# Kernel tuning notes

Measured on AMD Instinct MI355X. Metric: run time of the kernel, lower is better.

Reference implementation:

```python
import jax, jax.numpy as jnp
import numpy as np

EPS = 1e-5

def group_points(feat, idx):
    # feat: [B, C, N1], idx: [B, N2, K] -> [B, C, N2, K]
    return jax.vmap(lambda f, i: f[:, i])(feat, idx)

def conv_bn_relu(x, W, gamma, beta):
    # 1x1 conv2d (no bias) + training-mode BatchNorm2d + ReLU
    y = jnp.einsum('oc,bcnk->bonk', W, x)
    mean = y.mean(axis=(0, 2, 3), keepdims=True)
    var = y.var(axis=(0, 2, 3), keepdims=True)  # biased, as BN uses for normalization
    y = (y - mean) * jax.lax.rsqrt(var + EPS)
    y = y * gamma[None, :, None, None] + beta[None, :, None, None]
    return jax.nn.relu(y)

def setup_inputs() -> dict:
    key = jax.random.key(0)
    ks = jax.random.split(key, 12)
    B, N1, N2, K, C1 = 16, 4096, 1024, 32, 64
    mlp = [C1 + 3, 64, 64, 128]  # use_xyz adds 3 channels
    inp = {
        'in_xyz': jax.random.normal(ks[0], (B, 3, N1), jnp.float32),
        'out_xyz': jax.random.normal(ks[1], (B, 3, N2), jnp.float32),
        'in_feature': jax.random.normal(ks[2], (B, C1, N1), jnp.float32),
        'nbr_index': jax.random.randint(ks[3], (B, N2, K), 0, N1, jnp.int32),
    }
    for li in range(3):
        cin, cout = mlp[li], mlp[li + 1]
        inp[f'W{li}'] = jax.random.normal(ks[4 + li], (cout, cin), jnp.float32) * (1.0 / np.sqrt(cin))
        inp[f'g{li}'] = jnp.ones((cout,), jnp.float32)
        inp[f'b{li}'] = jnp.zeros((cout,), jnp.float32)
    return inp

def reference(in_xyz, out_xyz, in_feature, nbr_index,
              W0, g0, b0, W1, g1, b1, W2, g2, b2):
    # gather neighbor features: [B, C1, N2, K]
    nbr_feature = group_points(in_feature, nbr_index)
    # gather neighbor xyz, recenter on query points: [B, 3, N2, K]
    nbr_xyz = group_points(in_xyz, nbr_index) - out_xyz[:, :, :, None]
    x = jnp.concatenate([nbr_feature, nbr_xyz], axis=1)  # [B, C1+3, N2, K]
    x = conv_bn_relu(x, W0, g0, b0)
    x = conv_bn_relu(x, W1, g1, b1)
    x = conv_bn_relu(x, W2, g2, b2)
    return jnp.max(x, axis=3)  # [B, C2, N2]
```

## Files before the change

### kernel.cpp

```cpp
#include <hip/hip_runtime.h>
#include <cstdint>

typedef unsigned short u16;
typedef unsigned int   u32;
typedef __attribute__((ext_vector_type(8))) short  short8;
typedef __attribute__((ext_vector_type(4))) float  floatx4;
typedef __attribute__((ext_vector_type(4))) unsigned int u32x4;

#define NPTS 524288
#define NREP 4

__device__ __forceinline__ float b2f(u16 h) { return __uint_as_float(((u32)h) << 16); }
__device__ __forceinline__ u16 f2b(float f) {
  u32 u = __float_as_uint(f);
  return (u16)((u + 0x7FFFu + ((u >> 16) & 1u)) >> 16);
}
__device__ __forceinline__ u32 pk_bf16(float lo, float hi) {
  return (u32)f2b(lo) | ((u32)f2b(hi) << 16);
}
__device__ __forceinline__ short8 ld_frag8(const u16* p) {
  union { uint4 q; short8 s; } x;
  x.q = *(const uint4*)p;
  return x.s;
}
__device__ __forceinline__ short8 u4_to_s8(uint4 q) {
  union { uint4 q; short8 s; } x; x.q = q; return x.s;
}
__device__ __forceinline__ u32x4 nt_ld4(const void* p) {
  return __builtin_nontemporal_load((const u32x4*)p);
}

__global__ __launch_bounds__(256) void prep_all(const float* __restrict__ inf,
                                                const float* __restrict__ ixyz,
                                                const float* __restrict__ W0,
                                                const float* __restrict__ W1,
                                                const float* __restrict__ W2,
                                                u16* __restrict__ featT,
                                                u16* __restrict__ xyzB,
                                                u16* __restrict__ Wb,
                                                float* __restrict__ gz) {
  __shared__ float tile[32 * 33];
  const int bk = blockIdx.x, t = threadIdx.x;
  if (bk < 4096) {
    int b = bk >> 8, rem = bk & 255, cc = rem >> 7, nc = rem & 127;
    #pragma unroll
    for (int i = 0; i < 4; ++i) {
      int flat = t + i * 256;
      int cl = flat >> 5, nl = flat & 31;
      tile[cl * 33 + nl] = inf[(size_t)((b * 64) + cc * 32 + cl) * 4096 + nc * 32 + nl];
    }
    __syncthreads();
    #pragma unroll
    for (int i = 0; i < 4; ++i) {
      int flat = t + i * 256;
      int nl = flat >> 5, cl = flat & 31;
      featT[(size_t)((b << 12) + nc * 32 + nl) * 64 + cc * 32 + cl] = f2b(tile[cl * 33 + nl]);
    }
  } else if (bk < 4352) {
    int g = (bk - 4096) * 256 + t;
    int b = g >> 12, n = g & 4095;
    const float* p = ixyz + (size_t)b * 12288;
    u32 lo = pk_bf16(p[n], p[4096 + n]);
    u32 hi = (u32)f2b(p[8192 + n]);
    *(uint2*)(xyzB + (size_t)g * 4) = make_uint2(lo, hi);
  } else if (bk < 4432) {
    int s = (bk - 4352) * 256 + t;
    u16 v = 0;
    if (s < 6656)       { int o = s / 104, c = s % 104; if (c < 67) v = f2b(W0[o * 67 + c]); }
    else if (s < 11264) { int q = s - 6656;  int o = q / 72, c = q % 72; if (c < 64) v = f2b(W1[o * 64 + c]); }
    else                { int q = s - 11264; int o = q / 72, c = q % 72; if (c < 64) v = f2b(W2[o * 64 + c]); }
    Wb[s] = v;
  } else {
    #pragma unroll
    for (int i = 0; i < 8; ++i) gz[t + i * 256] = 0.f;
  }
}

template<int KSTEPS, int OCH, bool GATHER, bool MAXOUT>
__global__ __launch_bounds__(256, MAXOUT ? 4 : 5) void gemm_layer(
    const u16* __restrict__ xsrc, const u16* __restrict__ xyzB,
    const float* __restrict__ oxyz, const int* __restrict__ nbr,
    const u16* __restrict__ Wb,
    const float* __restrict__ gsin, const float* __restrict__ gam,
    const float* __restrict__ bet,
    u16* __restrict__ yout, u32* __restrict__ gm,
    float* __restrict__ gsout) {
  constexpr int PITCH = KSTEPS * 32 + 8;
  __shared__ __align__(16) u16 wsh[OCH * PITCH];
  __shared__ float red[512];
  __shared__ float ss[GATHER ? 4 : 128];
  __shared__ float corr[GATHER ? 8 : 1][64];
  __shared__ __align__(16) u32 xt[MAXOUT ? 256 : 2304];

  const int t = threadIdx.x;
  const int blk = (blockIdx.x & 7) * 256 + (blockIdx.x >> 3);
  const int lane = t & 63, wv = t >> 6, lr = lane & 15, quad = lane >> 4;
  const int P0 = blk * 256;
  const int b = blk >> 7;

  {
    const u32* src = (const u32*)Wb;
    u32* dst = (u32*)wsh;
    constexpr int NW = OCH * PITCH / 2;
    #pragma unroll
    for (int i = 0; i < NW / 256; ++i) dst[t + i * 256] = src[t + i * 256];
  }
  if constexpr (GATHER) {
    #pragma unroll
    for (int half = 0; half < 2; ++half) {
      int e = t + half * 256, nn = e >> 6, och = e & 63;
      int n2 = (blk * 8 + nn) & 1023;
      float c = 0.f;
      #pragma unroll
      for (int k = 0; k < 3; ++k)
        c += b2f(Wb[och * 104 + 64 + k]) * oxyz[((b * 3 + k) << 10) + n2];
      corr[nn][och] = c;
    }
  } else {
    if (t < 64) {
      float a = 0.f, q = 0.f;
      #pragma unroll
      for (int rep = 0; rep < NREP; ++rep) {
        a += gsin[rep * 128 + t];
        q += gsin[rep * 128 + 64 + t];
      }
      const float invN = 1.f / (float)NPTS;
      float mean = a * invN;
      float var  = fmaxf(q * invN - mean * mean, 0.f);
      float sc = gam[t] * rsqrtf(var + 1e-5f);
      ss[t] = sc; ss[64 + t] = bet[t] - mean * sc;
    }
  }
  __syncthreads();

  float scr[2][8], shr[2][8];
  if constexpr (!GATHER) {
    #pragma unroll
    for (int ks = 0; ks < 2; ++ks)
      #pragma unroll
      for (int i = 0; i < 8; ++i) {
        const int c = ks * 32 + quad * 8 + i;
        scr[ks][i] = ss[c]; shr[ks][i] = ss[64 + c];
      }
  }

  float s1[4] = {0.f, 0.f, 0.f, 0.f}, s2[4] = {0.f, 0.f, 0.f, 0.f};
  u32* yo = (u32*)yout;

  if constexpr (!MAXOUT) {
    const u16* bp = wsh + lr * PITCH + quad * 8;
    #pragma unroll
    for (int sub = 0; sub < 4; ++sub) {
      const int R = P0 + sub * 64 + wv * 16 + lr;
      short8 av[KSTEPS];
      if constexpr (GATHER) {
        const int id = __builtin_nontemporal_load(&nbr[R]);
        const u16* row = xsrc + (size_t)((b << 12) + id) * 64;
        uint4 a0 = *(const uint4*)(row + quad * 8);
        uint4 a1 = *(const uint4*)(row + quad * 8 + 32);
        u32 w0 = 0u, w1 = 0u;
        if (quad == 0) {
          uint2 v = *(const uint2*)(xyzB + (size_t)((b << 12) + id) * 4);
          w0 = v.x; w1 = v.y;
        }
        av[0] = u4_to_s8(a0);
        av[1] = u4_to_s8(a1);
        av[2] = u4_to_s8(make_uint4(w0, w1, 0u, 0u));
      } else {
        const u16* row = xsrc + ((size_t)R << 6);
        #pragma unroll
        for (int ks = 0; ks < KSTEPS; ++ks) {
          u32x4 raw = nt_ld4(row + ks * 32 + quad * 8);
          u32 w[4] = { raw[0], raw[1], raw[2], raw[3] };
          u32 o[4];
          #pragma unroll
          for (int j = 0; j < 4; ++j) {
            float lo = fmaxf(b2f((u16)(w[j] & 0xffffu)) * scr[ks][2 * j]     + shr[ks][2 * j],     0.f);
            float hi = fmaxf(b2f((u16)(w[j] >> 16))     * scr[ks][2 * j + 1] + shr[ks][2 * j + 1], 0.f);
            o[j] = pk_bf16(lo, hi);
          }
          av[ks] = u4_to_s8(make_uint4(o[0], o[1], o[2], o[3]));
        }
      }
      floatx4 acc[4];
      #pragma unroll
      for (int nt = 0; nt < 4; ++nt) acc[nt] = (floatx4){0.f, 0.f, 0.f, 0.f};
      #pragma unroll
      for (int ks = 0; ks < KSTEPS; ++ks)
        #pragma unroll
        for (int nt = 0; nt < 4; ++nt) {
          short8 bv = ld_frag8(bp + nt * 16 * PITCH + ks * 32);
          acc[nt] = __builtin_amdgcn_mfma_f32_16x16x32_bf16(av[ks], bv, acc[nt], 0, 0, 0);
        }
      float corrv[4] = {0.f, 0.f, 0.f, 0.f};
      if constexpr (GATHER) {
        const int nn = sub * 2 + (wv >> 1);
        #pragma unroll
        for (int nt = 0; nt < 4; ++nt) corrv[nt] = corr[nn][nt * 16 + lr];
      }
      #pragma unroll
      for (int nt = 0; nt < 4; ++nt)
        #pragma unroll
        for (int r = 0; r < 4; ++r) {
          float v = acc[nt][r] - corrv[nt];
          s1[nt] += v; s2[nt] += v * v;
          float vo = __shfl_xor(v, 1);
          if ((lr & 1) == 0)
            xt[(wv * 16 + quad * 4 + r) * 36 + nt * 8 + (lr >> 1)] = pk_bf16(v, vo);
        }
      __syncthreads();
      #pragma unroll
      for (int j = 0; j < 2; ++j) {
        int flat = t + j * 256;
        int rowb = flat >> 3, c4 = flat & 7;
        u32x4 q = *(const u32x4*)&xt[rowb * 36 + c4 * 4];
        __builtin_nontemporal_store(q, (u32x4*)&yo[(size_t)(P0 + sub * 64 + rowb) * 32 + c4 * 4]);
      }
      __syncthreads();
    }
  } else {
    const int rg = wv >> 1, cg = wv & 1;
    const u16* bp = wsh + (cg * 64 + lr) * PITCH + quad * 8;
    u32* gmt = xt + wv * 64;
    for (int sub = 0; sub < 4; ++sub) {
      short8 av[2][2];
      #pragma unroll
      for (int h = 0; h < 2; ++h) {
        const int R = P0 + sub * 64 + rg * 32 + h * 16 + lr;
        const u16* row = xsrc + ((size_t)R << 6);
        #pragma unroll
        for (int ks = 0; ks < 2; ++ks) {
          u32x4 raw = nt_ld4(row + ks * 32 + quad * 8);
          u32 w[4] = { raw[0], raw[1], raw[2], raw[3] };
          u32 o[4];
          #pragma unroll
          for (int j = 0; j < 4; ++j) {
            float lo = fmaxf(b2f((u16)(w[j] & 0xffffu)) * scr[ks][2 * j]     + shr[ks][2 * j],     0.f);
            float hi = fmaxf(b2f((u16)(w[j] >> 16))     * scr[ks][2 * j + 1] + shr[ks][2 * j + 1], 0.f);
            o[j] = pk_bf16(lo, hi);
          }
          av[h][ks] = u4_to_s8(make_uint4(o[0], o[1], o[2], o[3]));
        }
      }
      floatx4 acc[2][4];
      #pragma unroll
      for (int h = 0; h < 2; ++h)
        #pragma unroll
        for (int nt = 0; nt < 4; ++nt) acc[h][nt] = (floatx4){0.f, 0.f, 0.f, 0.f};
      #pragma unroll
      for (int ks = 0; ks < 2; ++ks)
        #pragma unroll
        for (int nt = 0; nt < 4; ++nt) {
          short8 bv = ld_frag8(bp + nt * 16 * PITCH + ks * 32);
          #pragma unroll
          for (int h = 0; h < 2; ++h)
            acc[h][nt] = __builtin_amdgcn_mfma_f32_16x16x32_bf16(av[h][ks], bv, acc[h][nt], 0, 0, 0);
        }
      float mx[4], mn[4];
      #pragma unroll
      for (int nt = 0; nt < 4; ++nt) {
        mx[nt] = -INFINITY; mn[nt] = INFINITY;
        #pragma unroll
        for (int h = 0; h < 2; ++h)
          #pragma unroll
          for (int r = 0; r < 4; ++r) {
            float v = acc[h][nt][r];
            s1[nt] += v; s2[nt] += v * v;
            mx[nt] = fmaxf(mx[nt], v); mn[nt] = fminf(mn[nt], v);
          }
        mx[nt] = fmaxf(mx[nt], __shfl_xor(mx[nt], 16));
        mx[nt] = fmaxf(mx[nt], __shfl_xor(mx[nt], 32));
        mn[nt] = fminf(mn[nt], __shfl_xor(mn[nt], 16));
        mn[nt] = fminf(mn[nt], __shfl_xor(mn[nt], 32));
      }
      if (lane < 16) {
        #pragma unroll
        for (int nt = 0; nt < 4; ++nt)
          gmt[nt * 16 + lane] = pk_bf16(mx[nt], mn[nt]);
      }
      __syncthreads();
      const int grp = blk * 8 + sub * 2 + rg;
      gm[(size_t)grp * 128 + cg * 64 + lane] = gmt[lane];
      __syncthreads();
    }
  }

  #pragma unroll
  for (int nt = 0; nt < 4; ++nt) {
    s1[nt] += __shfl_xor(s1[nt], 16); s1[nt] += __shfl_xor(s1[nt], 32);
    s2[nt] += __shfl_xor(s2[nt], 16); s2[nt] += __shfl_xor(s2[nt], 32);
  }
  if (lane < 16) {
    #pragma unroll
    for (int nt = 0; nt < 4; ++nt) {
      red[wv * 64 + nt * 16 + lr] = s1[nt];
      red[256 + wv * 64 + nt * 16 + lr] = s2[nt];
    }
  }
  __syncthreads();
  float* gb = gsout + (blk & (NREP - 1)) * (MAXOUT ? 256 : 128);
  if constexpr (!MAXOUT) {
    if (t < 64) {
      unsafeAtomicAdd(&gb[t], red[t] + red[64 + t] + red[128 + t] + red[192 + t]);
    } else if (t < 128) {
      int c = t - 64;
      unsafeAtomicAdd(&gb[64 + c], red[256 + c] + red[320 + c] + red[384 + c] + red[448 + c]);
    }
  } else {
    if (t < 128) {
      int half = t >> 6, i = t & 63;
      unsafeAtomicAdd(&gb[t], red[half * 64 + i] + red[(half + 2) * 64 + i]);
    } else {
      int c = t - 128, half = c >> 6, i = c & 63;
      unsafeAtomicAdd(&gb[128 + c], red[256 + half * 64 + i] + red[256 + (half + 2) * 64 + i]);
    }
  }
}

__global__ __launch_bounds__(256) void final_out(const u32* __restrict__ gm,
                                                 const float* __restrict__ gs,
                                                 const float* __restrict__ gam,
                                                 const float* __restrict__ bet,
                                                 float* __restrict__ out) {
  __shared__ float tile[64 * 33];
  __shared__ float ssc[128], ssh[128];
  int blk = blockIdx.x;
  int b = blk >> 6, rem = blk & 63, cc = rem >> 4, nn = rem & 15;
  int t = threadIdx.x;
  if (t < 128) {
    float a = 0.f, q = 0.f;
    #pragma unroll
    for (int rep = 0; rep < NREP; ++rep) {
      a += gs[rep * 256 + t];
      q += gs[rep * 256 + 128 + t];
    }
    const float invN = 1.f / (float)NPTS;
    float mean = a * invN;
    float var  = fmaxf(q * invN - mean * mean, 0.f);
    float sc = gam[t] * rsqrtf(var + 1e-5f);
    ssc[t] = sc; ssh[t] = bet[t] - mean * sc;
  }
  __syncthreads();
  #pragma unroll
  for (int i = 0; i < 8; ++i) {
    int flat = t + i * 256;
    int n2l = flat >> 5, cl = flat & 31;
    int c = cc * 32 + cl;
    size_t idx = (size_t)((b << 10) + nn * 64 + n2l) * 128 + c;
    u32 p = gm[idx];
    float mxv = b2f((u16)(p & 0xffffu)), mnv = b2f((u16)(p >> 16));
    float scv = ssc[c], shv = ssh[c];
    float v = (scv >= 0.f) ? mxv : mnv;
    tile[n2l * 33 + cl] = fmaxf(scv * v + shv, 0.f);
  }
  __syncthreads();
  #pragma unroll
  for (int i = 0; i < 8; ++i) {
    int flat = t + i * 256;
    int cl = flat >> 6, n2l = flat & 63;
    out[(size_t)((b * 128) + cc * 32 + cl) * 1024 + nn * 64 + n2l] = tile[n2l * 33 + cl];
  }
}

extern "C" void kernel_launch(void* const* d_in, const int* in_sizes, int n_in,
                              void* d_out, int out_size, void* d_ws, size_t ws_size,
                              hipStream_t stream) {
  const float* in_xyz  = (const float*)d_in[0];
  const float* out_xyz = (const float*)d_in[1];
  const float* in_feat = (const float*)d_in[2];
  const int*   nbr     = (const int*)d_in[3];
  const float* W0 = (const float*)d_in[4];
  const float* g0 = (const float*)d_in[5];
  const float* b0 = (const float*)d_in[6];
  const float* W1 = (const float*)d_in[7];
  const float* g1 = (const float*)d_in[8];
  const float* b1 = (const float*)d_in[9];
  const float* W2 = (const float*)d_in[10];
  const float* g2 = (const float*)d_in[11];
  const float* b2 = (const float*)d_in[12];
  float* out = (float*)d_out;

  char* ws = (char*)d_ws;
  u16*    Wb    = (u16*)(ws + 4096);
  float*  gs0   = (float*)(ws + 49152);
  float*  gs1   = (float*)(ws + 51200);
  float*  gs2   = (float*)(ws + 53248);
  u16*    featT = (u16*)(ws + 262144);
  u16*    xyzB  = (u16*)(ws + 8650752);
  u16*    y0    = (u16*)(ws + 9699328);
  u16*    y1    = (u16*)(ws + 76808192);
  u32*    gm    = (u32*)(ws + 9699328);

  hipLaunchKernelGGL(prep_all, dim3(4433), dim3(256), 0, stream,
                     in_feat, in_xyz, W0, W1, W2, featT, xyzB, Wb, gs0);

  hipLaunchKernelGGL((gemm_layer<3, 64, true, false>), dim3(2048), dim3(256), 0, stream,
                     featT, xyzB, out_xyz, nbr, Wb, nullptr, nullptr, nullptr,
                     y0, nullptr, gs0);

  hipLaunchKernelGGL((gemm_layer<2, 64, false, false>), dim3(2048), dim3(256), 0, stream,
                     y0, nullptr, nullptr, nullptr, Wb + 6656, gs0, g0, b0,
                     y1, nullptr, gs1);

  hipLaunchKernelGGL((gemm_layer<2, 128, false, true>), dim3(2048), dim3(256), 0, stream,
                     y1, nullptr, nullptr, nullptr, Wb + 11264, gs1, g1, b1,
                     nullptr, gm, gs2);

  hipLaunchKernelGGL(final_out, dim3(1024), dim3(256), 0, stream, gm, gs2, g2, b2, out);
}
```

Baseline: 214.9 us.

## Prefetch all sub-tile input rows up front and use lightweight LDS barriers

```diff
diff --git a/kernel.cpp b/kernel.cpp
--- a/kernel.cpp
+++ b/kernel.cpp
@@ -28,6 +28,9 @@
 }
 __device__ __forceinline__ u32x4 nt_ld4(const void* p) {
   return __builtin_nontemporal_load((const u32x4*)p);
+}
+__device__ __forceinline__ void bar_lds() {
+  asm volatile("s_waitcnt lgkmcnt(0)\n\ts_barrier" ::: "memory");
 }
 
 __global__ __launch_bounds__(256) void prep_all(const float* __restrict__ inf,
@@ -149,29 +152,42 @@
 
   if constexpr (!MAXOUT) {
     const u16* bp = wsh + lr * PITCH + quad * 8;
+    uint4 ga[4][2]; uint2 gx[4]; u32x4 raw[4][2];
+    if constexpr (GATHER) {
+      int idx4[4];
+      #pragma unroll
+      for (int sub = 0; sub < 4; ++sub)
+        idx4[sub] = __builtin_nontemporal_load(&nbr[P0 + sub * 64 + wv * 16 + lr]);
+      #pragma unroll
+      for (int sub = 0; sub < 4; ++sub) {
+        const u16* row = xsrc + (size_t)((b << 12) + idx4[sub]) * 64;
+        ga[sub][0] = *(const uint4*)(row + quad * 8);
+        ga[sub][1] = *(const uint4*)(row + quad * 8 + 32);
+        if (quad == 0)
+          gx[sub] = *(const uint2*)(xyzB + (size_t)((b << 12) + idx4[sub]) * 4);
+      }
+    } else {
+      #pragma unroll
+      for (int sub = 0; sub < 4; ++sub) {
+        const u16* row = xsrc + ((size_t)(P0 + sub * 64 + wv * 16 + lr) << 6);
+        #pragma unroll
+        for (int ks = 0; ks < 2; ++ks)
+          raw[sub][ks] = nt_ld4(row + ks * 32 + quad * 8);
+      }
+    }
     #pragma unroll
     for (int sub = 0; sub < 4; ++sub) {
-      const int R = P0 + sub * 64 + wv * 16 + lr;
       short8 av[KSTEPS];
       if constexpr (GATHER) {
-        const int id = __builtin_nontemporal_load(&nbr[R]);
-        const u16* row = xsrc + (size_t)((b << 12) + id) * 64;
-        uint4 a0 = *(const uint4*)(row + quad * 8);
-        uint4 a1 = *(const uint4*)(row + quad * 8 + 32);
         u32 w0 = 0u, w1 = 0u;
-        if (quad == 0) {
-          uint2 v = *(const uint2*)(xyzB + (size_t)((b << 12) + id) * 4);
-          w0 = v.x; w1 = v.y;
-        }
-        av[0] = u4_to_s8(a0);
-        av[1] = u4_to_s8(a1);
+        if (quad == 0) { w0 = gx[sub].x; w1 = gx[sub].y; }
+        av[0] = u4_to_s8(ga[sub][0]);
+        av[1] = u4_to_s8(ga[sub][1]);
         av[2] = u4_to_s8(make_uint4(w0, w1, 0u, 0u));
       } else {
-        const u16* row = xsrc + ((size_t)R << 6);
-        #pragma unroll
-        for (int ks = 0; ks < KSTEPS; ++ks) {
-          u32x4 raw = nt_ld4(row + ks * 32 + quad * 8);
-          u32 w[4] = { raw[0], raw[1], raw[2], raw[3] };
+        #pragma unroll
+        for (int ks = 0; ks < 2; ++ks) {
+          u32 w[4] = { raw[sub][ks][0], raw[sub][ks][1], raw[sub][ks][2], raw[sub][ks][3] };
           u32 o[4];
           #pragma unroll
           for (int j = 0; j < 4; ++j) {
@@ -208,30 +224,38 @@
           if ((lr & 1) == 0)
             xt[(wv * 16 + quad * 4 + r) * 36 + nt * 8 + (lr >> 1)] = pk_bf16(v, vo);
         }
-      __syncthreads();
+      bar_lds();
       #pragma unroll
       for (int j = 0; j < 2; ++j) {
         int flat = t + j * 256;
         int rowb = flat >> 3, c4 = flat & 7;
         u32x4 q = *(const u32x4*)&xt[rowb * 36 + c4 * 4];
-        __builtin_nontemporal_store(q, (u32x4*)&yo[(size_t)(P0 + sub * 64 + rowb) * 32 + c4 * 4]);
-      }
-      __syncthreads();
+        *(u32x4*)&yo[(size_t)(P0 + sub * 64 + rowb) * 32 + c4 * 4] = q;
+      }
+      bar_lds();
     }
   } else {
     const int rg = wv >> 1, cg = wv & 1;
     const u16* bp = wsh + (cg * 64 + lr) * PITCH + quad * 8;
     u32* gmt = xt + wv * 64;
+    u32x4 raw[4][2][2];
+    #pragma unroll
+    for (int sub = 0; sub < 4; ++sub)
+      #pragma unroll
+      for (int h = 0; h < 2; ++h) {
+        const u16* row = xsrc + ((size_t)(P0 + sub * 64 + rg * 32 + h * 16 + lr) << 6);
+        #pragma unroll
+        for (int ks = 0; ks < 2; ++ks)
+          raw[sub][h][ks] = nt_ld4(row + ks * 32 + quad * 8);
+      }
+    #pragma unroll
     for (int sub = 0; sub < 4; ++sub) {
       short8 av[2][2];
       #pragma unroll
-      for (int h = 0; h < 2; ++h) {
-        const int R = P0 + sub * 64 + rg * 32 + h * 16 + lr;
-        const u16* row = xsrc + ((size_t)R << 6);
+      for (int h = 0; h < 2; ++h)
         #pragma unroll
         for (int ks = 0; ks < 2; ++ks) {
-          u32x4 raw = nt_ld4(row + ks * 32 + quad * 8);
-          u32 w[4] = { raw[0], raw[1], raw[2], raw[3] };
+          u32 w[4] = { raw[sub][h][ks][0], raw[sub][h][ks][1], raw[sub][h][ks][2], raw[sub][h][ks][3] };
           u32 o[4];
           #pragma unroll
           for (int j = 0; j < 4; ++j) {
@@ -241,7 +265,6 @@
           }
           av[h][ks] = u4_to_s8(make_uint4(o[0], o[1], o[2], o[3]));
         }
-      }
       floatx4 acc[2][4];
       #pragma unroll
       for (int h = 0; h < 2; ++h)
@@ -278,10 +301,10 @@
         for (int nt = 0; nt < 4; ++nt)
           gmt[nt * 16 + lane] = pk_bf16(mx[nt], mn[nt]);
       }
-      __syncthreads();
+      bar_lds();
       const int grp = blk * 8 + sub * 2 + rg;
       gm[(size_t)grp * 128 + cg * 64 + lane] = gmt[lane];
-      __syncthreads();
+      bar_lds();
     }
   }
 
```

After: 246.9 us. +14.9%, slower.
